# Optimization experiments

Hardware: AMD Instinct MI355X
Metric: run time of the kernel (lower is better)

The kernel has to match this reference:

```python
import jax, jax.numpy as jnp
import numpy as np

H = 16      # num heads
DH = 64     # head dim
D = H * DH  # hidden = 1024

def setup_inputs() -> dict:
    key = jax.random.key(0)
    ks = jax.random.split(key, 8)
    B, S = 4, 2048
    scale = 1.0 / np.sqrt(D)
    return {
        "hidden_states": jax.random.normal(ks[0], (B, S, D), dtype=jnp.float32),
        "attention_mask": jnp.zeros((B, S, S), dtype=jnp.float32),
        "Wq": jax.random.normal(ks[1], (D, D), dtype=jnp.float32) * scale,
        "bq": jnp.zeros((D,), dtype=jnp.float32),
        "Wk": jax.random.normal(ks[2], (D, D), dtype=jnp.float32) * scale,
        "bk": jnp.zeros((D,), dtype=jnp.float32),
        "Wv": jax.random.normal(ks[3], (D, D), dtype=jnp.float32) * scale,
        "bv": jnp.zeros((D,), dtype=jnp.float32),
    }

def _split_heads(x):
    B, S, _ = x.shape
    return x.reshape(B, S, H, DH).transpose(0, 2, 1, 3)  # [B,H,S,dh]

def reference(hidden_states, attention_mask, Wq, bq, Wk, bk, Wv, bv):
    q = _split_heads(hidden_states @ Wq + bq)
    k = _split_heads(hidden_states @ Wk + bk)
    v = _split_heads(hidden_states @ Wv + bv)
    scores = jnp.einsum("bhqd,bhkd->bhqk", q, k) / jnp.sqrt(jnp.float32(DH))
    scores = scores + attention_mask[:, None, :, :]
    probs = jax.nn.softmax(scores, axis=-1)  # dropout p=0 (eval) -> identity
    ctx = jnp.einsum("bhqk,bhkd->bhqd", probs, v)
    B, _, S, _ = ctx.shape
    return ctx.transpose(0, 2, 1, 3).reshape(B, S, H * DH)
```

## Files before the change

### kernel.cpp

```cpp
#include <hip/hip_runtime.h>

typedef __bf16 bf16;
typedef __bf16 bf16x8 __attribute__((ext_vector_type(8)));
typedef __bf16 bf16x4 __attribute__((ext_vector_type(4)));
typedef float floatx4 __attribute__((ext_vector_type(4)));

typedef __attribute__((address_space(1))) void gvoid;
typedef __attribute__((address_space(3))) void lvoid;
#define ASYNC_COPY16(gp, lp) \
  __builtin_amdgcn_global_load_lds((gvoid*)(gp), (lvoid*)(lp), 16, 0, 0)

#define NB 4
#define SQ 2048
#define DMODEL 1024
#define NH 16
#define HD 64
#define MTOK (NB * SQ)
#define LOG2E 1.44269504088896f

#define XB_OFF 0ull
#define WT_OFF (16ull * 1024 * 1024)
#define Q_OFF  (22ull * 1024 * 1024)
#define K_OFF  (38ull * 1024 * 1024)
#define V_OFF  (54ull * 1024 * 1024)
#define FLG_OFF (70ull * 1024 * 1024)

__global__ __launch_bounds__(256) void prep(
    const float* __restrict__ x, bf16* __restrict__ xb,
    const float* __restrict__ w0, const float* __restrict__ w1,
    const float* __restrict__ w2, bf16* __restrict__ wt,
    const float* __restrict__ mask, int* __restrict__ flags) {
  __shared__ float tlds[32][33];
  int blk = blockIdx.x;
  int t = threadIdx.x;
  if (blk < 8192) {
    int i = blk * 256 + t;
    float4 v = ((const float4*)x)[i];
    bf16x4 o;
    o[0] = (bf16)v.x; o[1] = (bf16)v.y; o[2] = (bf16)v.z; o[3] = (bf16)v.w;
    ((bf16x4*)xb)[i] = o;
  } else if (blk < 11264) {
    int tidx = blk - 8192;
    int z = tidx >> 10;
    int rem = tidx & 1023;
    int kb = ((rem >> 5) & 31) * 32, nb = (rem & 31) * 32;
    const float* w = (z == 0) ? w0 : (z == 1) ? w1 : w2;
    bf16* out = wt + (size_t)z * DMODEL * DMODEL;
    int tx = t & 31, ty = t >> 5;
#pragma unroll
    for (int i = 0; i < 4; i++)
      tlds[ty + 8 * i][tx] = w[(size_t)(kb + ty + 8 * i) * DMODEL + nb + tx];
    __syncthreads();
#pragma unroll
    for (int i = 0; i < 4; i++)
      out[(size_t)(nb + ty + 8 * i) * DMODEL + kb + tx] = (bf16)tlds[tx][ty + 8 * i];
  } else {
    int midx = blk - 11264;
    int kt = midx & 31, qt = (midx >> 5) & 15, b = midx >> 9;
    const float* mb = mask + ((size_t)b * SQ + qt * 128) * SQ + kt * 64;
    int row = t >> 1, half = t & 1;
    const float4* p = (const float4*)(mb + (size_t)row * SQ + half * 32);
    bool nz = false;
#pragma unroll
    for (int i = 0; i < 8; i++) {
      float4 vv = p[i];
      nz |= (vv.x != 0.f) | (vv.y != 0.f) | (vv.z != 0.f) | (vv.w != 0.f);
    }
    int* acc = (int*)tlds;
    if (t == 0) acc[0] = 0;
    __syncthreads();
    unsigned long long m = __ballot(nz);
    if ((t & 63) == 0 && m) atomicOr(acc, 1);
    __syncthreads();
    if (t == 0) flags[(b * 16 + qt) * 32 + kt] = acc[0];
  }
}

#define BK 64
__global__ __launch_bounds__(256) void qkv(
    const bf16* __restrict__ xb,
    const bf16* __restrict__ wt,
    const float* __restrict__ biasq, const float* __restrict__ biask,
    const float* __restrict__ biasv,
    bf16* __restrict__ q, bf16* __restrict__ k, bf16* __restrict__ v) {
  __shared__ bf16 As[128 * BK];
  __shared__ bf16 Bs[128 * BK];

  int id = blockIdx.x;
  int local = id >> 3;
  int mt = ((id & 7) << 3) | (local & 7);
  int nt = local >> 3;
  int t = threadIdx.x;

  int mat = nt >> 3;
  int nbase = (nt & 7) * 128;
  const bf16* wmat = wt + (size_t)mat * DMODEL * DMODEL;
  const float* bias = (mat == 0) ? biasq : (mat == 1) ? biask : biasv;
  bf16* outp = (mat == 0) ? q : (mat == 1) ? k : v;

  int lane = t & 63, wid = t >> 6;
  int quad = lane >> 4, l16 = lane & 15;
  int wm = (wid & 1) * 64, wn = (wid >> 1) * 64;
  int xq = quad ^ (l16 & 7);

  floatx4 acc[4][4] = {};

  for (int kb = 0; kb < DMODEL; kb += BK) {
    __syncthreads();
#pragma unroll
    for (int p = 0; p < 4; p++) {
      int i2 = p * 256 + t;
      int row = i2 >> 3;
      int gch = (i2 ^ row) & 7;
      ASYNC_COPY16(xb + (size_t)(mt * 128 + row) * DMODEL + kb + gch * 8,
                   As + i2 * 8);
      ASYNC_COPY16(wmat + (size_t)(nbase + row) * DMODEL + kb + gch * 8,
                   Bs + i2 * 8);
    }
    __syncthreads();

#pragma unroll
    for (int kc = 0; kc < BK; kc += 32) {
      int xc = (kc >> 3) ^ xq;
      bf16x8 af[4], bfr[4];
#pragma unroll
      for (int mi = 0; mi < 4; mi++)
        af[mi] = *(const bf16x8*)(As + (wm + mi * 16 + l16) * BK + xc * 8);
#pragma unroll
      for (int ni = 0; ni < 4; ni++)
        bfr[ni] = *(const bf16x8*)(Bs + (wn + ni * 16 + l16) * BK + xc * 8);
      if (mat < 2) {
#pragma unroll
        for (int mi = 0; mi < 4; mi++)
#pragma unroll
          for (int ni = 0; ni < 4; ni++)
            acc[mi][ni] = __builtin_amdgcn_mfma_f32_16x16x32_bf16(
                bfr[ni], af[mi], acc[mi][ni], 0, 0, 0);
      } else {
#pragma unroll
        for (int mi = 0; mi < 4; mi++)
#pragma unroll
          for (int ni = 0; ni < 4; ni++)
            acc[mi][ni] = __builtin_amdgcn_mfma_f32_16x16x32_bf16(
                af[mi], bfr[ni], acc[mi][ni], 0, 0, 0);
      }
    }
  }

  int mg0 = mt * 128 + wm;
  if (mat < 2) {
    float qscale = (mat == 0) ? 0.125f * LOG2E : 1.0f;
#pragma unroll
    for (int ni = 0; ni < 4; ni++) {
      int n0 = nbase + wn + ni * 16 + quad * 4;
      int h = n0 >> 6, d0 = n0 & 63;
      float4 bv4 = *(const float4*)(bias + n0);
#pragma unroll
      for (int mi = 0; mi < 4; mi++) {
        int m = mg0 + mi * 16 + l16;
        int b = m >> 11, s = m & 2047;
        bf16x4 pk;
        pk[0] = (bf16)((acc[mi][ni][0] + bv4.x) * qscale);
        pk[1] = (bf16)((acc[mi][ni][1] + bv4.y) * qscale);
        pk[2] = (bf16)((acc[mi][ni][2] + bv4.z) * qscale);
        pk[3] = (bf16)((acc[mi][ni][3] + bv4.w) * qscale);
        *(bf16x4*)(outp + (((size_t)(b * NH + h) * SQ + s) << 6) + d0) = pk;
      }
    }
  } else {
#pragma unroll
    for (int ni = 0; ni < 4; ni++) {
      int n = nbase + wn + ni * 16 + l16;
      int h = n >> 6, d = n & 63;
      float bv_ = bias[n];
#pragma unroll
      for (int mi = 0; mi < 4; mi++) {
        int m0 = mg0 + mi * 16 + quad * 4;
        int b = m0 >> 11, s = m0 & 2047;
        bf16x4 pk;
#pragma unroll
        for (int r = 0; r < 4; r++) pk[r] = (bf16)(acc[mi][ni][r] + bv_);
        *(bf16x4*)(outp + (((size_t)(b * NH + h) * HD + d) << 11) + s) = pk;
      }
    }
  }
}

#define PPAD 72
__global__ __launch_bounds__(256, 4) void attn(
    const bf16* __restrict__ Q,
    const bf16* __restrict__ K,
    const bf16* __restrict__ Vt,
    const float* __restrict__ mask,
    const int* __restrict__ flags,
    float* __restrict__ out) {
  __shared__ bf16 Ks[64 * 64];
  __shared__ bf16 Vs[64 * 64];
  __shared__ bf16 P[4][32][PPAD];

  int bh = blockIdx.x;
  int qt = blockIdx.y;
  int b = bh >> 4, h = bh & 15;
  int t = threadIdx.x, lane = t & 63, wid = t >> 6;
  int quad = lane >> 4, l16 = lane & 15;
  int q0 = qt * 128 + wid * 32;

  const bf16* Qp = Q + ((size_t)bh * SQ + q0) * HD;
  const bf16* Kp = K + (size_t)bh * SQ * HD;
  const bf16* Vp = Vt + (size_t)bh * HD * SQ;
  const float* mp = mask + ((size_t)b * SQ + q0) * SQ;
  const int* flg = flags + (b * 16 + qt) * 32;

  bf16x8 qa[2][2];
#pragma unroll
  for (int m = 0; m < 2; m++) {
    const bf16* qr = Qp + (size_t)(m * 16 + l16) * HD;
    qa[m][0] = *(const bf16x8*)(qr + quad * 8);
    qa[m][1] = *(const bf16x8*)(qr + 32 + quad * 8);
  }

  floatx4 o[2][4] = {};
  float li[2] = {0.f, 0.f};
  bf16* Pw = &P[wid][0][0];
  int xq = quad ^ (l16 & 7);

  for (int kb = 0, kti = 0; kb < SQ; kb += 64, kti++) {
    __syncthreads();
#pragma unroll
    for (int p = 0; p < 2; p++) {
      int idx = p * 256 + t;
      int row = idx >> 3;
      int gch = (idx ^ row) & 7;
      ASYNC_COPY16(Kp + (size_t)(kb + row) * HD + gch * 8, Ks + idx * 8);
      ASYNC_COPY16(Vp + (size_t)row * SQ + kb + gch * 8, Vs + idx * 8);
    }
    __syncthreads();
    int flag = flg[kti];

    float xs[2][4][4];
    __builtin_amdgcn_s_setprio(1);
#pragma unroll
    for (int kt = 0; kt < 4; kt++) {
      const bf16* kr = Ks + (kt * 16 + l16) * 64;
      bf16x8 k0 = *(const bf16x8*)(kr + xq * 8);
      bf16x8 k1 = *(const bf16x8*)(kr + (xq ^ 4) * 8);
      floatx4 z0 = {}, z1 = {};
      z0 = __builtin_amdgcn_mfma_f32_16x16x32_bf16(k0, qa[0][0], z0, 0, 0, 0);
      z0 = __builtin_amdgcn_mfma_f32_16x16x32_bf16(k1, qa[0][1], z0, 0, 0, 0);
      z1 = __builtin_amdgcn_mfma_f32_16x16x32_bf16(k0, qa[1][0], z1, 0, 0, 0);
      z1 = __builtin_amdgcn_mfma_f32_16x16x32_bf16(k1, qa[1][1], z1, 0, 0, 0);
#pragma unroll
      for (int r = 0; r < 4; r++) { xs[0][kt][r] = z0[r]; xs[1][kt][r] = z1[r]; }
    }
    __builtin_amdgcn_s_setprio(0);
    if (flag) {
#pragma unroll
      for (int m = 0; m < 2; m++)
#pragma unroll
        for (int kt = 0; kt < 4; kt++)
#pragma unroll
          for (int r = 0; r < 4; r++)
            xs[m][kt][r] = __builtin_fmaf(
                mp[(size_t)(m * 16 + l16) * SQ + kb + kt * 16 + quad * 4 + r],
                LOG2E, xs[m][kt][r]);
    }

#pragma unroll
    for (int m = 0; m < 2; m++) {
      float sum = 0.f;
#pragma unroll
      for (int kt = 0; kt < 4; kt++) {
        bf16x4 pk;
#pragma unroll
        for (int r = 0; r < 4; r++) {
          float e = __builtin_amdgcn_exp2f(xs[m][kt][r]);
          sum += e;
          pk[r] = (bf16)e;
        }
        *(bf16x4*)(Pw + (m * 16 + l16) * PPAD + kt * 16 + quad * 4) = pk;
      }
      li[m] += sum;
    }
    asm volatile("s_waitcnt lgkmcnt(0)" ::: "memory");
    bf16x8 pb[2][2];
#pragma unroll
    for (int m = 0; m < 2; m++) {
      pb[m][0] = *(const bf16x8*)(Pw + (m * 16 + l16) * PPAD + quad * 8);
      pb[m][1] = *(const bf16x8*)(Pw + (m * 16 + l16) * PPAD + 32 + quad * 8);
    }

    __builtin_amdgcn_s_setprio(1);
#pragma unroll
    for (int dt = 0; dt < 4; dt++) {
      const bf16* vr = Vs + (dt * 16 + l16) * 64;
      bf16x8 v0 = *(const bf16x8*)(vr + xq * 8);
      bf16x8 v1 = *(const bf16x8*)(vr + (xq ^ 4) * 8);
      o[0][dt] = __builtin_amdgcn_mfma_f32_16x16x32_bf16(v0, pb[0][0], o[0][dt], 0, 0, 0);
      o[0][dt] = __builtin_amdgcn_mfma_f32_16x16x32_bf16(v1, pb[0][1], o[0][dt], 0, 0, 0);
      o[1][dt] = __builtin_amdgcn_mfma_f32_16x16x32_bf16(v0, pb[1][0], o[1][dt], 0, 0, 0);
      o[1][dt] = __builtin_amdgcn_mfma_f32_16x16x32_bf16(v1, pb[1][1], o[1][dt], 0, 0, 0);
    }
    __builtin_amdgcn_s_setprio(0);
  }
#pragma unroll
  for (int m = 0; m < 2; m++) {
    li[m] += __shfl_xor(li[m], 16, 64);
    li[m] += __shfl_xor(li[m], 32, 64);
  }
#pragma unroll
  for (int m = 0; m < 2; m++) {
    float inv = 1.0f / li[m];
    float* op = out + ((size_t)b * SQ + q0 + m * 16 + l16) * DMODEL + h * HD;
#pragma unroll
    for (int dt = 0; dt < 4; dt++)
#pragma unroll
      for (int r = 0; r < 4; r++)
        op[dt * 16 + quad * 4 + r] = o[m][dt][r] * inv;
  }
}

extern "C" void kernel_launch(void* const* d_in, const int* in_sizes, int n_in,
                              void* d_out, int out_size, void* d_ws, size_t ws_size,
                              hipStream_t stream) {
  (void)in_sizes; (void)n_in; (void)out_size; (void)ws_size;
  const float* hs   = (const float*)d_in[0];
  const float* mask = (const float*)d_in[1];
  const float* Wq   = (const float*)d_in[2];
  const float* bq   = (const float*)d_in[3];
  const float* Wk   = (const float*)d_in[4];
  const float* bk   = (const float*)d_in[5];
  const float* Wv   = (const float*)d_in[6];
  const float* bv   = (const float*)d_in[7];
  float* out = (float*)d_out;
  char* ws = (char*)d_ws;
  bf16* xb = (bf16*)(ws + XB_OFF);
  bf16* wt = (bf16*)(ws + WT_OFF);
  bf16* q  = (bf16*)(ws + Q_OFF);
  bf16* k  = (bf16*)(ws + K_OFF);
  bf16* v  = (bf16*)(ws + V_OFF);
  int* flg = (int*)(ws + FLG_OFF);

  prep<<<8192 + 3072 + 2048, 256, 0, stream>>>(hs, xb, Wq, Wk, Wv, wt, mask, flg);
  qkv<<<1536, 256, 0, stream>>>(xb, wt, bq, bk, bv, q, k, v);
  attn<<<dim3(64, 16), 256, 0, stream>>>(q, k, v, mask, flg, out);
}
```

Before: 301.8 us.

## Double-buffer K/V tiles in attention and XOR-swizzle the P scratch buffer

The attention kernel now keeps two LDS buffers each for K and V. It prefetches the next 64-key tile with async global-to-LDS copies while the current tile runs through QK^T, softmax and PV, which removes the second barrier per iteration and hides load latency behind compute. The padded per-wave P buffer is replaced by an unpadded layout with an XOR swizzle on 8-element chunks, to avoid LDS bank conflicts without the padding. LDS use per block grows, so the launch bound drops from 4 to 3 blocks per CU, trading some occupancy for overlap.

```diff
diff --git a/kernel.cpp b/kernel.cpp
--- a/kernel.cpp
+++ b/kernel.cpp
@@ -186,17 +186,16 @@
   }
 }
 
-#define PPAD 72
-__global__ __launch_bounds__(256, 4) void attn(
+__global__ __launch_bounds__(256, 3) void attn(
     const bf16* __restrict__ Q,
     const bf16* __restrict__ K,
     const bf16* __restrict__ Vt,
     const float* __restrict__ mask,
     const int* __restrict__ flags,
     float* __restrict__ out) {
-  __shared__ bf16 Ks[64 * 64];
-  __shared__ bf16 Vs[64 * 64];
-  __shared__ bf16 P[4][32][PPAD];
+  __shared__ bf16 Ks[2][64 * 64];
+  __shared__ bf16 Vs[2][64 * 64];
+  __shared__ bf16 P[4][32 * 64];
 
   int bh = blockIdx.x;
   int qt = blockIdx.y;
@@ -221,27 +220,43 @@
 
   floatx4 o[2][4] = {};
   float li[2] = {0.f, 0.f};
-  bf16* Pw = &P[wid][0][0];
+  bf16* Pw = &P[wid][0];
   int xq = quad ^ (l16 & 7);
-
-  for (int kb = 0, kti = 0; kb < SQ; kb += 64, kti++) {
-    __syncthreads();
-#pragma unroll
-    for (int p = 0; p < 2; p++) {
-      int idx = p * 256 + t;
-      int row = idx >> 3;
-      int gch = (idx ^ row) & 7;
-      ASYNC_COPY16(Kp + (size_t)(kb + row) * HD + gch * 8, Ks + idx * 8);
-      ASYNC_COPY16(Vp + (size_t)row * SQ + kb + gch * 8, Vs + idx * 8);
-    }
-    __syncthreads();
+  int ps = l16 & 7;
+
+#pragma unroll
+  for (int p = 0; p < 2; p++) {
+    int idx = p * 256 + t;
+    int row = idx >> 3;
+    int gch = (idx ^ row) & 7;
+    ASYNC_COPY16(Kp + (size_t)row * HD + gch * 8, Ks[0] + idx * 8);
+    ASYNC_COPY16(Vp + (size_t)row * SQ + gch * 8, Vs[0] + idx * 8);
+  }
+
+  int cur = 0;
+  for (int kb = 0, kti = 0; kb < SQ; kb += 64, kti++, cur ^= 1) {
+    __syncthreads();
+    if (kb + 64 < SQ) {
+#pragma unroll
+      for (int p = 0; p < 2; p++) {
+        int idx = p * 256 + t;
+        int row = idx >> 3;
+        int gch = (idx ^ row) & 7;
+        ASYNC_COPY16(Kp + (size_t)(kb + 64 + row) * HD + gch * 8,
+                     Ks[cur ^ 1] + idx * 8);
+        ASYNC_COPY16(Vp + (size_t)row * SQ + kb + 64 + gch * 8,
+                     Vs[cur ^ 1] + idx * 8);
+      }
+    }
     int flag = flg[kti];
+    const bf16* Kc = Ks[cur];
+    const bf16* Vc = Vs[cur];
 
     float xs[2][4][4];
     __builtin_amdgcn_s_setprio(1);
 #pragma unroll
     for (int kt = 0; kt < 4; kt++) {
-      const bf16* kr = Ks + (kt * 16 + l16) * 64;
+      const bf16* kr = Kc + (kt * 16 + l16) * 64;
       bf16x8 k0 = *(const bf16x8*)(kr + xq * 8);
       bf16x8 k1 = *(const bf16x8*)(kr + (xq ^ 4) * 8);
       floatx4 z0 = {}, z1 = {};
@@ -268,6 +283,7 @@
 #pragma unroll
     for (int m = 0; m < 2; m++) {
       float sum = 0.f;
+      bf16* prow = Pw + (m * 16 + l16) * 64;
 #pragma unroll
       for (int kt = 0; kt < 4; kt++) {
         bf16x4 pk;
@@ -277,7 +293,8 @@
           sum += e;
           pk[r] = (bf16)e;
         }
-        *(bf16x4*)(Pw + (m * 16 + l16) * PPAD + kt * 16 + quad * 4) = pk;
+        int u = 2 * kt + (quad >> 1);
+        *(bf16x4*)(prow + ((u ^ ps) * 8) + (quad & 1) * 4) = pk;
       }
       li[m] += sum;
     }
@@ -285,14 +302,15 @@
     bf16x8 pb[2][2];
 #pragma unroll
     for (int m = 0; m < 2; m++) {
-      pb[m][0] = *(const bf16x8*)(Pw + (m * 16 + l16) * PPAD + quad * 8);
-      pb[m][1] = *(const bf16x8*)(Pw + (m * 16 + l16) * PPAD + 32 + quad * 8);
+      const bf16* prow = Pw + (m * 16 + l16) * 64;
+      pb[m][0] = *(const bf16x8*)(prow + (quad ^ ps) * 8);
+      pb[m][1] = *(const bf16x8*)(prow + ((quad + 4) ^ ps) * 8);
     }
 
     __builtin_amdgcn_s_setprio(1);
 #pragma unroll
     for (int dt = 0; dt < 4; dt++) {
-      const bf16* vr = Vs + (dt * 16 + l16) * 64;
+      const bf16* vr = Vc + (dt * 16 + l16) * 64;
       bf16x8 v0 = *(const bf16x8*)(vr + xq * 8);
       bf16x8 v1 = *(const bf16x8*)(vr + (xq ^ 4) * 8);
       o[0][dt] = __builtin_amdgcn_mfma_f32_16x16x32_bf16(v0, pb[0][0], o[0][dt], 0, 0, 0);
```

Result: slower. 309.0 us (+2.4%).

## Rearrange softmax probabilities in registers with permlane swaps instead of LDS round-trip

Applied to the files above, without the earlier changes.

Removes the per-wave shared-memory P buffer. Probabilities are packed to bf16 with v_cvt_pk_bf16_f32 and redistributed across lanes with v_permlane32/16_swap so they already sit in the MFMA B-operand layout. This drops the LDS write/read and the lgkmcnt wait from every key block, and the smaller LDS footprint lets launch bounds rise from 4 to 6 blocks per CU. The risk is that the lane permutation does not exactly match the original P layout, and the tighter launch bound may cause register spills.

```diff
diff --git a/kernel.cpp b/kernel.cpp
--- a/kernel.cpp
+++ b/kernel.cpp
@@ -4,6 +4,7 @@
 typedef __bf16 bf16x8 __attribute__((ext_vector_type(8)));
 typedef __bf16 bf16x4 __attribute__((ext_vector_type(4)));
 typedef float floatx4 __attribute__((ext_vector_type(4)));
+typedef unsigned int uint4t __attribute__((ext_vector_type(4)));
 
 typedef __attribute__((address_space(1))) void gvoid;
 typedef __attribute__((address_space(3))) void lvoid;
@@ -186,8 +187,7 @@
   }
 }
 
-#define PPAD 72
-__global__ __launch_bounds__(256, 4) void attn(
+__global__ __launch_bounds__(256, 6) void attn(
     const bf16* __restrict__ Q,
     const bf16* __restrict__ K,
     const bf16* __restrict__ Vt,
@@ -196,7 +196,6 @@
     float* __restrict__ out) {
   __shared__ bf16 Ks[64 * 64];
   __shared__ bf16 Vs[64 * 64];
-  __shared__ bf16 P[4][32][PPAD];
 
   int bh = blockIdx.x;
   int qt = blockIdx.y;
@@ -221,7 +220,6 @@
 
   floatx4 o[2][4] = {};
   float li[2] = {0.f, 0.f};
-  bf16* Pw = &P[wid][0][0];
   int xq = quad ^ (l16 & 7);
 
   for (int kb = 0, kti = 0; kb < SQ; kb += 64, kti++) {
@@ -265,28 +263,34 @@
                 LOG2E, xs[m][kt][r]);
     }
 
+    bf16x8 pb[2][2];
 #pragma unroll
     for (int m = 0; m < 2; m++) {
       float sum = 0.f;
+      unsigned int u[4][2];
 #pragma unroll
       for (int kt = 0; kt < 4; kt++) {
-        bf16x4 pk;
-#pragma unroll
-        for (int r = 0; r < 4; r++) {
-          float e = __builtin_amdgcn_exp2f(xs[m][kt][r]);
-          sum += e;
-          pk[r] = (bf16)e;
-        }
-        *(bf16x4*)(Pw + (m * 16 + l16) * PPAD + kt * 16 + quad * 4) = pk;
+        float e0 = __builtin_amdgcn_exp2f(xs[m][kt][0]);
+        float e1 = __builtin_amdgcn_exp2f(xs[m][kt][1]);
+        float e2 = __builtin_amdgcn_exp2f(xs[m][kt][2]);
+        float e3 = __builtin_amdgcn_exp2f(xs[m][kt][3]);
+        sum += (e0 + e1) + (e2 + e3);
+        asm("v_cvt_pk_bf16_f32 %0, %1, %2" : "=v"(u[kt][0]) : "v"(e0), "v"(e1));
+        asm("v_cvt_pk_bf16_f32 %0, %1, %2" : "=v"(u[kt][1]) : "v"(e2), "v"(e3));
       }
       li[m] += sum;
-    }
-    asm volatile("s_waitcnt lgkmcnt(0)" ::: "memory");
-    bf16x8 pb[2][2];
-#pragma unroll
-    for (int m = 0; m < 2; m++) {
-      pb[m][0] = *(const bf16x8*)(Pw + (m * 16 + l16) * PPAD + quad * 8);
-      pb[m][1] = *(const bf16x8*)(Pw + (m * 16 + l16) * PPAD + 32 + quad * 8);
+#pragma unroll
+      for (int f = 0; f < 2; f++) {
+        unsigned int a0 = u[2 * f][0], b0 = u[2 * f + 1][0];
+        unsigned int a1 = u[2 * f][1], b1 = u[2 * f + 1][1];
+        asm("v_permlane32_swap_b32 %0, %1" : "+v"(a0), "+v"(b0));
+        asm("v_permlane32_swap_b32 %0, %1" : "+v"(a1), "+v"(b1));
+        asm("v_permlane16_swap_b32 %0, %1" : "+v"(a0), "+v"(b0));
+        asm("v_permlane16_swap_b32 %0, %1" : "+v"(a1), "+v"(b1));
+        uint4t w;
+        w[0] = a0; w[1] = a1; w[2] = b0; w[3] = b1;
+        pb[m][f] = __builtin_bit_cast(bf16x8, w);
+      }
     }
 
     __builtin_amdgcn_s_setprio(1);
```

New measurement: 560.9 us. 1.86x slower.
